# Kernel tuning notes

Hardware: AMD Instinct MI355X
Metric: run time of the kernel (lower is better)

## Reference

```python
import jax, jax.numpy as jnp
import numpy as np

B, S, D, H = 2, 2048, 768, 12
DEPTH = D // H


def setup_inputs() -> dict:
    key = jax.random.key(0)
    ks = jax.random.split(key, 8)
    scale = 1.0 / np.sqrt(D)
    inp = {
        "query": jax.random.normal(ks[0], (B, S, D), jnp.float32),
        "key": jax.random.normal(ks[1], (B, S, D), jnp.float32),
        "value": jax.random.normal(ks[2], (B, S, D), jnp.float32),
        # additive mask convention: 1.0 where attention is disallowed (causal)
        "mask": jnp.triu(jnp.ones((1, 1, S, S), jnp.float32), k=1),
        "Wq": jax.random.normal(ks[3], (D, D), jnp.float32) * scale,
        "bq": jnp.zeros((D,), jnp.float32),
        "Wk": jax.random.normal(ks[4], (D, D), jnp.float32) * scale,
        "bk": jnp.zeros((D,), jnp.float32),
        "Wv": jax.random.normal(ks[5], (D, D), jnp.float32) * scale,
        "bv": jnp.zeros((D,), jnp.float32),
        "Wo": jax.random.normal(ks[6], (D, D), jnp.float32) * scale,
        "bo": jnp.zeros((D,), jnp.float32),
    }
    return inp


def _split_heads(x):
    # [B, S, D] -> [B, H, S, depth]
    b, s, _ = x.shape
    return x.reshape(b, s, H, DEPTH).transpose(0, 2, 1, 3)


def reference(query, key, value, mask, Wq, bq, Wk, bk, Wv, bv, Wo, bo):
    q = _split_heads(query @ Wq + bq)   # [B,H,S,depth]
    k = _split_heads(key @ Wk + bk)
    v = _split_heads(value @ Wv + bv)

    d_k = jnp.asarray(DEPTH, q.dtype)
    logits = jnp.einsum("bhqd,bhkd->bhqk", q, k) / jnp.sqrt(d_k)
    logits = logits + mask * -1e9
    weights = jax.nn.softmax(logits, axis=-1)          # [B,H,S,S] -- O(N^2)
    attn = jnp.einsum("bhqk,bhkd->bhqd", weights, v)    # [B,H,S,depth]

    concat = attn.transpose(0, 2, 1, 3).reshape(query.shape[0], -1, D)
    return concat @ Wo + bo
```

## Files before the change

kernel.cpp:

```cpp
#include <hip/hip_runtime.h>


typedef __bf16 bf16;
typedef __bf16 bf16x8 __attribute__((ext_vector_type(8)));
typedef __bf16 bf16x4 __attribute__((ext_vector_type(4)));
typedef float  f32x4  __attribute__((ext_vector_type(4)));

__device__ __forceinline__ void async_load16(const void* g, void* l) {
  __builtin_amdgcn_global_load_lds(
      (__attribute__((address_space(1))) void*)g,
      (__attribute__((address_space(3))) void*)l, 16, 0, 0);
}

__constant__ unsigned char chunk_tab[40] = {
  3, 4, 5, 6, 7, 8, 9, 10, 11, 12, 13, 14, 15,
  7 | 16, 8 | 16, 9 | 16, 10 | 16, 11 | 16, 12 | 16, 13 | 16, 14 | 16, 15 | 16,
  11 | 32, 12 | 32, 13 | 32, 14 | 32, 15 | 32,
  15 | 48,
  2, 6 | 16, 10 | 32, 14 | 48,
  1, 5 | 16, 9 | 32, 13 | 48,
  0, 4 | 16, 8 | 32, 12 | 48,
};

__global__ __launch_bounds__(256) void convert_kernel(
    const float* __restrict__ q, const float* __restrict__ k,
    const float* __restrict__ v, bf16* __restrict__ qo,
    bf16* __restrict__ ko, bf16* __restrict__ vo) {
  const float* src; bf16* dst;
  if (blockIdx.y == 0)      { src = q; dst = qo; }
  else if (blockIdx.y == 1) { src = k; dst = ko; }
  else                      { src = v; dst = vo; }
  size_t i = ((size_t)blockIdx.x * 256 + threadIdx.x) * 8;
  f32x4 a = *(const f32x4*)(src + i);
  f32x4 b = *(const f32x4*)(src + i + 4);
  bf16x8 o;
  o[0]=(bf16)a[0]; o[1]=(bf16)a[1]; o[2]=(bf16)a[2]; o[3]=(bf16)a[3];
  o[4]=(bf16)b[0]; o[5]=(bf16)b[1]; o[6]=(bf16)b[2]; o[7]=(bf16)b[3];
  *(bf16x8*)(dst + i) = o;
}

__global__ __launch_bounds__(256) void transpose_w_kernel(
    const float* __restrict__ W0, const float* __restrict__ W1,
    const float* __restrict__ W2, const float* __restrict__ W3,
    bf16* __restrict__ T0, bf16* __restrict__ T1,
    bf16* __restrict__ T2, bf16* __restrict__ T3) {
  const float* W; bf16* T;
  switch (blockIdx.z) {
    case 0: W = W0; T = T0; break;
    case 1: W = W1; T = T1; break;
    case 2: W = W2; T = T2; break;
    default: W = W3; T = T3; break;
  }
  __shared__ float tile[32][33];
  const int tx = threadIdx.x, ty = threadIdx.y;
  const int k0 = blockIdx.y * 32, n0 = blockIdx.x * 32;
#pragma unroll
  for (int j = 0; j < 32; j += 8)
    tile[ty + j][tx] = W[(size_t)(k0 + ty + j) * 768 + n0 + tx];
  __syncthreads();
#pragma unroll
  for (int j = 0; j < 32; j += 8) {
    int n = ty + j;
    T[(size_t)(n0 + n) * 768 + k0 + tx] = (bf16)tile[tx][n];
  }
}

__global__ __launch_bounds__(256, 4) void gemm_qkv_kernel(
    const bf16* __restrict__ A0, const bf16* __restrict__ A1, const bf16* __restrict__ A2,
    const bf16* __restrict__ W0, const bf16* __restrict__ W1, const bf16* __restrict__ W2,
    const float* __restrict__ b0, const float* __restrict__ b1, const float* __restrict__ b2,
    bf16* __restrict__ Q, bf16* __restrict__ K, bf16* __restrict__ V) {
  __shared__ __align__(16) char smem[32768];
  const int bidx = blockIdx.x;
  const int xcd = bidx & 7, ii = bidx >> 3;
  const int nt = ii % 6, mzi = ii / 6;
  const int mz = mzi * 8 + xcd;
  const int m = mz & 31, z = mz >> 5;
  const int m0 = m * 128, n0 = nt * 128;

  const bf16* A    = (z == 0) ? A0 : (z == 1) ? A1 : A2;
  const bf16* Wt   = (z == 0) ? W0 : (z == 1) ? W1 : W2;
  const float* bias = (z == 0) ? b0 : (z == 1) ? b1 : b2;
  bf16* outb = (z == 0) ? Q : (z == 1) ? K : V;
  const int mode = (z == 2) ? 1 : 0;

  const int t = threadIdx.x;
  const int w = t >> 6, lane = t & 63;
  const int wm = w >> 1, wn = w & 1;
  const int quad = lane >> 4, l15 = lane & 15;
  const int srow = lane >> 3, k8p = lane & 7;

  size_t offA[4], offB[4];
  int ldsOff[4];
#pragma unroll
  for (int i = 0; i < 4; ++i) {
    const int rl = w * 32 + i * 8 + srow;
    const int kk = k8p ^ (rl & 7);
    offA[i] = (size_t)(m0 + rl) * 768 + kk * 8;
    offB[i] = (size_t)(n0 + rl) * 768 + kk * 8;
    ldsOff[i] = (w * 32 + i * 8) * 128;
  }

  f32x4 acc[4][4] = {};

  for (int kidx = 0; kidx < 12; ++kidx) {
    const int k1 = kidx * 64;
#pragma unroll
    for (int i = 0; i < 4; ++i) {
      async_load16(A  + offA[i] + k1, smem + ldsOff[i]);
      async_load16(Wt + offB[i] + k1, smem + 16384 + ldsOff[i]);
    }
    __syncthreads();
    const bf16* As = (const bf16*)smem;
    const bf16* Bs = (const bf16*)(smem + 16384);
#pragma unroll
    for (int ks = 0; ks < 2; ++ks) {
      bf16x8 af[4], bfv[4];
      const int slot = (((ks * 4 + quad) ^ (lane & 7)) * 8);
#pragma unroll
      for (int mi = 0; mi < 4; ++mi)
        af[mi] = *(const bf16x8*)(As + (wm * 64 + mi * 16 + l15) * 64 + slot);
#pragma unroll
      for (int ni = 0; ni < 4; ++ni)
        bfv[ni] = *(const bf16x8*)(Bs + (wn * 64 + ni * 16 + l15) * 64 + slot);
#pragma unroll
      for (int mi = 0; mi < 4; ++mi)
#pragma unroll
        for (int ni = 0; ni < 4; ++ni)
          acc[mi][ni] = __builtin_amdgcn_mfma_f32_16x16x32_bf16(af[mi], bfv[ni], acc[mi][ni], 0, 0, 0);
    }
    __syncthreads();
  }

#pragma unroll
  for (int ni = 0; ni < 4; ++ni) {
    const float bc = bias[n0 + wn * 64 + ni * 16 + l15];
#pragma unroll
    for (int mi = 0; mi < 4; ++mi)
#pragma unroll
      for (int r = 0; r < 4; ++r) acc[mi][ni][r] += bc;
  }

  if (mode == 0) {
    bf16* Ce = (bf16*)smem;
#pragma unroll
    for (int hh = 0; hh < 2; ++hh) {
      if (wm == hh) {
#pragma unroll
        for (int ni = 0; ni < 4; ++ni) {
          const int col = wn * 64 + ni * 16 + l15;
#pragma unroll
          for (int mi = 0; mi < 4; ++mi) {
            const int row = mi * 16 + quad * 4;
#pragma unroll
            for (int r = 0; r < 4; ++r)
              Ce[(row + r) * 136 + col] = (bf16)acc[mi][ni][r];
          }
        }
      }
      __syncthreads();
#pragma unroll
      for (int j = 0; j < 4; ++j) {
        const int ci = j * 256 + t;
        const int row = ci >> 4, c8 = (ci & 15) * 8;
        bf16x8 vv = *(const bf16x8*)(Ce + row * 136 + c8);
        const int rg = m0 + hh * 64 + row, cg = n0 + c8;
        const int bb = rg >> 11, s = rg & 2047;
        const int h = cg >> 6, d = cg & 63;
        *(bf16x8*)(outb + ((size_t)(bb * 12 + h) * 2048 + s) * 64 + d) = vv;
      }
      __syncthreads();
    }
  } else {
    bf16* Ct = (bf16*)smem;
#pragma unroll
    for (int hh = 0; hh < 2; ++hh) {
      if (wm == hh) {
#pragma unroll
        for (int ni = 0; ni < 4; ++ni) {
          const int col = wn * 64 + ni * 16 + l15;
#pragma unroll
          for (int mi = 0; mi < 4; ++mi) {
            const int row = mi * 16 + quad * 4;
            bf16x4 pv;
            pv[0] = (bf16)acc[mi][ni][0]; pv[1] = (bf16)acc[mi][ni][1];
            pv[2] = (bf16)acc[mi][ni][2]; pv[3] = (bf16)acc[mi][ni][3];
            *(bf16x4*)(Ct + (size_t)col * 72 + row) = pv;
          }
        }
      }
      __syncthreads();
#pragma unroll
      for (int j = 0; j < 4; ++j) {
        const int ci = j * 256 + t;
        const int col = ci >> 3, r8 = (ci & 7) * 8;
        bf16x8 vv = *(const bf16x8*)(Ct + col * 72 + r8);
        const int cg = n0 + col;
        const int h = cg >> 6, d = cg & 63;
        const int rg = m0 + hh * 64 + r8;
        const int bb = rg >> 11, s = rg & 2047;
        *(bf16x8*)(outb + ((size_t)(bb * 12 + h) * 64 + d) * 2048 + s) = vv;
      }
      __syncthreads();
    }
  }
}

__global__ __launch_bounds__(256, 4) void attn_kernel(
    const bf16* __restrict__ Qh, const bf16* __restrict__ Kh,
    const bf16* __restrict__ Vt,
    bf16* __restrict__ O0, bf16* __restrict__ O1,
    bf16* __restrict__ O2, bf16* __restrict__ O3,
    float* __restrict__ L0, float* __restrict__ L1,
    float* __restrict__ L2, float* __restrict__ L3) {
  const int ent = chunk_tab[blockIdx.x / 24];
  const int bh = blockIdx.x % 24;
  const int qt = ent & 15, c = ent >> 4;
  const int q0 = qt * 128;
  const int kt_begin = c * 8;
  const int ntiles = 2 * qt + 2;
  const int kt_end = (kt_begin + 8 < ntiles) ? kt_begin + 8 : ntiles;

  __shared__ __align__(16) char smem[32768];
  bf16* Ps = (bf16*)(smem + 16384);

  const int t = threadIdx.x;
  const int w = t >> 6, lane = t & 63, quad = lane >> 4, l15 = lane & 15;
  const int srow = lane >> 3, k8p = lane & 7;
  const bf16* Qp = Qh + (size_t)bh * (2048 * 64);
  const bf16* Kp = Kh + (size_t)bh * (2048 * 64);
  const bf16* Vp = Vt + (size_t)bh * (64 * 2048);

  size_t offK[2], offV[2];
  int ldsOff[2];
#pragma unroll
  for (int i = 0; i < 2; ++i) {
    const int rl = w * 16 + i * 8 + srow;
    const int kk = k8p ^ (rl & 7);
    offK[i] = (size_t)rl * 64 + kk * 8;
    offV[i] = (size_t)rl * 2048 + kk * 8;
    ldsOff[i] = (w * 16 + i * 8) * 128;
  }

  bf16x8 qf[2][2];
#pragma unroll
  for (int mi = 0; mi < 2; ++mi)
#pragma unroll
    for (int ks = 0; ks < 2; ++ks) {
      const int qrow = q0 + w * 32 + mi * 16 + l15;
      qf[mi][ks] = *(const bf16x8*)(Qp + (size_t)qrow * 64 + ks * 32 + quad * 8);
    }

  f32x4 o[2][4] = {};
  float lp[2] = {0.f, 0.f};
  const float sc = 0.125f * 1.44269504f;

  for (int kt = kt_begin; kt < kt_end; ++kt) {
    const int k0 = kt * 64;
#pragma unroll
    for (int i = 0; i < 2; ++i) {
      async_load16(Kp + offK[i] + (size_t)k0 * 64, smem + ldsOff[i]);
      async_load16(Vp + offV[i] + k0,              smem + 8192 + ldsOff[i]);
    }
    __syncthreads();
    const bf16* Ks = (const bf16*)smem;
    const bf16* Vs = (const bf16*)(smem + 8192);

    f32x4 st[4][2] = {};
#pragma unroll
    for (int ks = 0; ks < 2; ++ks) {
      const int slot = (((ks * 4 + quad) ^ (lane & 7)) * 8);
      bf16x8 kf[4];
#pragma unroll
      for (int ni = 0; ni < 4; ++ni)
        kf[ni] = *(const bf16x8*)(Ks + (ni * 16 + l15) * 64 + slot);
#pragma unroll
      for (int ni = 0; ni < 4; ++ni)
#pragma unroll
        for (int mi = 0; mi < 2; ++mi)
          st[ni][mi] = __builtin_amdgcn_mfma_f32_16x16x32_bf16(kf[ni], qf[mi][ks], st[ni][mi], 0, 0, 0);
    }

    const bool diag = (k0 + 63 > q0);
#pragma unroll
    for (int mi = 0; mi < 2; ++mi) {
      const int q_local = w * 32 + mi * 16 + l15;
      const int qg = q0 + q_local;
#pragma unroll
      for (int ni = 0; ni < 4; ++ni) {
        bf16x4 pv;
#pragma unroll
        for (int r = 0; r < 4; ++r) {
          float p = __builtin_amdgcn_exp2f(st[ni][mi][r] * sc);
          if (diag && (k0 + ni * 16 + quad * 4 + r > qg)) p = 0.0f;
          lp[mi] += p;
          pv[r] = (bf16)p;
        }
        const int cc = ni * 2 + (quad >> 1);
        *(bf16x4*)(Ps + q_local * 64 + ((cc ^ (q_local & 7)) << 3) + ((quad & 1) << 2)) = pv;
      }
    }

#pragma unroll
    for (int ks = 0; ks < 2; ++ks) {
      const int slot = (((ks * 4 + quad) ^ (lane & 7)) * 8);
      bf16x8 pf[2], vfr[4];
#pragma unroll
      for (int mi = 0; mi < 2; ++mi)
        pf[mi] = *(const bf16x8*)(Ps + (w * 32 + mi * 16 + l15) * 64 + slot);
#pragma unroll
      for (int di = 0; di < 4; ++di)
        vfr[di] = *(const bf16x8*)(Vs + (di * 16 + l15) * 64 + slot);
#pragma unroll
      for (int mi = 0; mi < 2; ++mi)
#pragma unroll
        for (int di = 0; di < 4; ++di)
          o[mi][di] = __builtin_amdgcn_mfma_f32_16x16x32_bf16(pf[mi], vfr[di], o[mi][di], 0, 0, 0);
    }
    __syncthreads();
  }

  bf16* Op; float* Lp_;
  switch (c) {
    case 0: Op = O0; Lp_ = L0; break;
    case 1: Op = O1; Lp_ = L1; break;
    case 2: Op = O2; Lp_ = L2; break;
    default: Op = O3; Lp_ = L3; break;
  }
  const int rows_c = 2048 - 512 * c;
  const size_t rbase = (size_t)bh * rows_c + (q0 - 512 * c);

#pragma unroll
  for (int mi = 0; mi < 2; ++mi) {
    float l = lp[mi];
    l += __shfl_xor(l, 16);
    l += __shfl_xor(l, 32);
    if (quad == 0) Lp_[rbase + w * 32 + mi * 16 + l15] = l;
#pragma unroll
    for (int di = 0; di < 4; ++di) {
      const int d = di * 16 + l15;
#pragma unroll
      for (int r = 0; r < 4; ++r) {
        const size_t row = rbase + w * 32 + mi * 16 + quad * 4 + r;
        Op[row * 64 + d] = (bf16)o[mi][di][r];
      }
    }
  }
}

__global__ __launch_bounds__(256) void lsum_kernel(
    const float* __restrict__ L0, const float* __restrict__ L1,
    const float* __restrict__ L2, const float* __restrict__ L3,
    float* __restrict__ Linv) {
  const int row = blockIdx.x * 256 + threadIdx.x;
  const int bh = row >> 11, s = row & 2047;
  float l = L0[row];
  if (s >= 512)  l += L1[(size_t)bh * 1536 + (s - 512)];
  if (s >= 1024) l += L2[(size_t)bh * 1024 + (s - 1024)];
  if (s >= 1536) l += L3[(size_t)bh * 512  + (s - 1536)];
  Linv[row] = 1.0f / l;
}

__global__ __launch_bounds__(256, 4) void gemm_out_kernel(
    const bf16* __restrict__ O0, const bf16* __restrict__ O1,
    const bf16* __restrict__ O2, const bf16* __restrict__ O3,
    const float* __restrict__ Linv, const bf16* __restrict__ Wt,
    const float* __restrict__ bias, float* __restrict__ out) {
  __shared__ __align__(16) char smem[24576];
  const int bidx = blockIdx.x;
  const int xcd = bidx & 7, ii = bidx >> 3;
  const int nt = ii % 6, mg = ii / 6;
  const int mt = mg * 8 + xcd;
  const int m0 = mt * 64, n0 = nt * 128;
  const int bb = mt >> 5;
  const int s0 = (mt & 31) * 64;
  const int nch = 1 + (s0 >= 512) + (s0 >= 1024) + (s0 >= 1536);

  const int t = threadIdx.x;
  const int w = t >> 6, lane = t & 63;
  const int wm = w >> 1, wn = w & 1;
  const int quad = lane >> 4, l15 = lane & 15;
  const int srow = lane >> 3, k8p = lane & 7;

  size_t offB[4]; int ldsOffB[4];
#pragma unroll
  for (int i = 0; i < 4; ++i) {
    const int rl = w * 32 + i * 8 + srow;
    const int kk = k8p ^ (rl & 7);
    offB[i] = (size_t)(n0 + rl) * 768 + kk * 8;
    ldsOffB[i] = (w * 32 + i * 8) * 128;
  }
  const int arow = t >> 2;
  const int ac2 = (t & 3) * 2;
  const int sA = s0 + arow;
  size_t ro0[2], ro1[2], ro2[2], ro3[2];
  int apos[2];
#pragma unroll
  for (int j = 0; j < 2; ++j) {
    const int cch = ac2 + j;
    ro0[j] = (size_t)sA * 64 + cch * 8;
    ro1[j] = (size_t)(sA - 512) * 64 + cch * 8;
    ro2[j] = (size_t)(sA - 1024) * 64 + cch * 8;
    ro3[j] = (size_t)(sA - 1536) * 64 + cch * 8;
    apos[j] = arow * 64 + ((cch ^ (arow & 7)) << 3);
  }

  f32x4 acc[2][4] = {};
  bf16x8 pa0[2], pa1[2], pa2[2], pa3[2];
  float lv;

  auto loadA = [&](int kk) {
    const size_t bh = (size_t)(bb * 12 + kk);
    lv = Linv[bh * 2048 + sA];
#pragma unroll
    for (int j = 0; j < 2; ++j) pa0[j] = *(const bf16x8*)(O0 + bh * 131072 + ro0[j]);
    if (nch >= 2)
#pragma unroll
      for (int j = 0; j < 2; ++j) pa1[j] = *(const bf16x8*)(O1 + bh * 98304 + ro1[j]);
    if (nch >= 3)
#pragma unroll
      for (int j = 0; j < 2; ++j) pa2[j] = *(const bf16x8*)(O2 + bh * 65536 + ro2[j]);
    if (nch >= 4)
#pragma unroll
      for (int j = 0; j < 2; ++j) pa3[j] = *(const bf16x8*)(O3 + bh * 32768 + ro3[j]);
  };
  auto writeA = [&]() {
    bf16* As = (bf16*)smem;
#pragma unroll
    for (int j = 0; j < 2; ++j) {
      float f[8];
#pragma unroll
      for (int k = 0; k < 8; ++k) f[k] = (float)pa0[j][k];
      if (nch >= 2)
#pragma unroll
        for (int k = 0; k < 8; ++k) f[k] += (float)pa1[j][k];
      if (nch >= 3)
#pragma unroll
        for (int k = 0; k < 8; ++k) f[k] += (float)pa2[j][k];
      if (nch >= 4)
#pragma unroll
        for (int k = 0; k < 8; ++k) f[k] += (float)pa3[j][k];
      bf16x8 o;
#pragma unroll
      for (int k = 0; k < 8; ++k) o[k] = (bf16)(f[k] * lv);
      *(bf16x8*)(As + apos[j]) = o;
    }
  };

  loadA(0);
  for (int kidx = 0; kidx < 12; ++kidx) {
    writeA();
    const int k1 = kidx * 64;
#pragma unroll
    for (int i = 0; i < 4; ++i)
      async_load16(Wt + offB[i] + k1, smem + 8192 + ldsOffB[i]);
    __syncthreads();
    if (kidx < 11) loadA(kidx + 1);
    const bf16* As = (const bf16*)smem;
    const bf16* Bs = (const bf16*)(smem + 8192);
#pragma unroll
    for (int ks = 0; ks < 2; ++ks) {
      bf16x8 af[2], bfv[4];
      const int slot = (((ks * 4 + quad) ^ (lane & 7)) * 8);
#pragma unroll
      for (int mi = 0; mi < 2; ++mi)
        af[mi] = *(const bf16x8*)(As + (wm * 32 + mi * 16 + l15) * 64 + slot);
#pragma unroll
      for (int ni = 0; ni < 4; ++ni)
        bfv[ni] = *(const bf16x8*)(Bs + (wn * 64 + ni * 16 + l15) * 64 + slot);
#pragma unroll
      for (int mi = 0; mi < 2; ++mi)
#pragma unroll
        for (int ni = 0; ni < 4; ++ni)
          acc[mi][ni] = __builtin_amdgcn_mfma_f32_16x16x32_bf16(af[mi], bfv[ni], acc[mi][ni], 0, 0, 0);
    }
    __syncthreads();
  }

#pragma unroll
  for (int ni = 0; ni < 4; ++ni) {
    const float bc = bias[n0 + wn * 64 + ni * 16 + l15];
#pragma unroll
    for (int mi = 0; mi < 2; ++mi)
#pragma unroll
      for (int r = 0; r < 4; ++r) acc[mi][ni][r] += bc;
  }

#pragma unroll
  for (int ni = 0; ni < 4; ++ni) {
    const int col = n0 + wn * 64 + ni * 16 + l15;
#pragma unroll
    for (int mi = 0; mi < 2; ++mi) {
      const int row = m0 + wm * 32 + mi * 16 + quad * 4;
#pragma unroll
      for (int r = 0; r < 4; ++r)
        out[(size_t)(row + r) * 768 + col] = acc[mi][ni][r];
    }
  }
}

extern "C" void kernel_launch(void* const* d_in, const int* in_sizes, int n_in,
                              void* d_out, int out_size, void* d_ws, size_t ws_size,
                              hipStream_t stream) {
  const float* query = (const float*)d_in[0];
  const float* key   = (const float*)d_in[1];
  const float* value = (const float*)d_in[2];
  const float* Wq = (const float*)d_in[4];
  const float* bq = (const float*)d_in[5];
  const float* Wk = (const float*)d_in[6];
  const float* bk = (const float*)d_in[7];
  const float* Wv = (const float*)d_in[8];
  const float* bv = (const float*)d_in[9];
  const float* Wo = (const float*)d_in[10];
  const float* bo = (const float*)d_in[11];
  float* out = (float*)d_out;

  char* ws = (char*)d_ws;
  bf16* qb   = (bf16*)(ws);
  bf16* kb   = (bf16*)(ws + 6291456);
  bf16* vb   = (bf16*)(ws + 12582912);
  bf16* O0   = (bf16*)(ws);
  bf16* O1   = (bf16*)(ws + 6291456);
  bf16* O2   = (bf16*)(ws + 11010048);
  bf16* O3   = (bf16*)(ws + 14155776);
  float* L0  = (float*)(ws + 15728640);
  float* L1  = (float*)(ws + 15925248);
  float* L2  = (float*)(ws + 16072704);
  float* L3  = (float*)(ws + 16171008);
  float* Liv = (float*)(ws + 16220160);
  bf16* wtq  = (bf16*)(ws + 18874368);
  bf16* wtk  = (bf16*)(ws + 20054016);
  bf16* wtv  = (bf16*)(ws + 21233664);
  bf16* wto  = (bf16*)(ws + 22413312);
  bf16* Qh   = (bf16*)(ws + 23592960);
  bf16* Kh   = (bf16*)(ws + 29884416);
  bf16* Vtb  = (bf16*)(ws + 36175872);

  convert_kernel<<<dim3(1536, 3), 256, 0, stream>>>(query, key, value, qb, kb, vb);
  transpose_w_kernel<<<dim3(24, 24, 4), dim3(32, 8), 0, stream>>>(Wq, Wk, Wv, Wo, wtq, wtk, wtv, wto);
  gemm_qkv_kernel<<<dim3(576), 256, 0, stream>>>(qb, kb, vb, wtq, wtk, wtv, bq, bk, bv, Qh, Kh, Vtb);
  attn_kernel<<<dim3(960), 256, 0, stream>>>(Qh, Kh, Vtb, O0, O1, O2, O3, L0, L1, L2, L3);
  lsum_kernel<<<dim3(192), 256, 0, stream>>>(L0, L1, L2, L3, Liv);
  gemm_out_kernel<<<dim3(384), 256, 0, stream>>>(O0, O1, O2, O3, Liv, wto, bo, out);
}
```

Baseline: 189.2 us.

## Fuse input conversion into QKV GEMM and row-sum into output GEMM

Removes the separate fp32→bf16 convert kernel by having the QKV GEMM load fp32 activations into registers and convert them while writing to LDS, with register prefetch of the next K tile. Likewise removes the lsum kernel by computing inverse row sums into shared memory at the start of the output GEMM. Replaces the async global-to-LDS loads with register-staged loads plus software prefetch in the GEMMs and the attention kernel. This cuts two launches and an intermediate round trip through memory, at the cost of more registers (occupancy hint lowered to 3) and more VALU conversion work inside the GEMM.

```diff
diff --git a/kernel.cpp b/kernel.cpp
--- a/kernel.cpp
+++ b/kernel.cpp
@@ -5,12 +5,6 @@
 typedef __bf16 bf16x8 __attribute__((ext_vector_type(8)));
 typedef __bf16 bf16x4 __attribute__((ext_vector_type(4)));
 typedef float  f32x4  __attribute__((ext_vector_type(4)));
-
-__device__ __forceinline__ void async_load16(const void* g, void* l) {
-  __builtin_amdgcn_global_load_lds(
-      (__attribute__((address_space(1))) void*)g,
-      (__attribute__((address_space(3))) void*)l, 16, 0, 0);
-}
 
 __constant__ unsigned char chunk_tab[40] = {
   3, 4, 5, 6, 7, 8, 9, 10, 11, 12, 13, 14, 15,
@@ -21,23 +15,6 @@
   1, 5 | 16, 9 | 32, 13 | 48,
   0, 4 | 16, 8 | 32, 12 | 48,
 };
-
-__global__ __launch_bounds__(256) void convert_kernel(
-    const float* __restrict__ q, const float* __restrict__ k,
-    const float* __restrict__ v, bf16* __restrict__ qo,
-    bf16* __restrict__ ko, bf16* __restrict__ vo) {
-  const float* src; bf16* dst;
-  if (blockIdx.y == 0)      { src = q; dst = qo; }
-  else if (blockIdx.y == 1) { src = k; dst = ko; }
-  else                      { src = v; dst = vo; }
-  size_t i = ((size_t)blockIdx.x * 256 + threadIdx.x) * 8;
-  f32x4 a = *(const f32x4*)(src + i);
-  f32x4 b = *(const f32x4*)(src + i + 4);
-  bf16x8 o;
-  o[0]=(bf16)a[0]; o[1]=(bf16)a[1]; o[2]=(bf16)a[2]; o[3]=(bf16)a[3];
-  o[4]=(bf16)b[0]; o[5]=(bf16)b[1]; o[6]=(bf16)b[2]; o[7]=(bf16)b[3];
-  *(bf16x8*)(dst + i) = o;
-}
 
 __global__ __launch_bounds__(256) void transpose_w_kernel(
     const float* __restrict__ W0, const float* __restrict__ W1,
@@ -65,8 +42,8 @@
   }
 }
 
-__global__ __launch_bounds__(256, 4) void gemm_qkv_kernel(
-    const bf16* __restrict__ A0, const bf16* __restrict__ A1, const bf16* __restrict__ A2,
+__global__ __launch_bounds__(256, 3) void gemm_qkv_kernel(
+    const float* __restrict__ X0, const float* __restrict__ X1, const float* __restrict__ X2,
     const bf16* __restrict__ W0, const bf16* __restrict__ W1, const bf16* __restrict__ W2,
     const float* __restrict__ b0, const float* __restrict__ b1, const float* __restrict__ b2,
     bf16* __restrict__ Q, bf16* __restrict__ K, bf16* __restrict__ V) {
@@ -78,8 +55,8 @@
   const int m = mz & 31, z = mz >> 5;
   const int m0 = m * 128, n0 = nt * 128;
 
-  const bf16* A    = (z == 0) ? A0 : (z == 1) ? A1 : A2;
-  const bf16* Wt   = (z == 0) ? W0 : (z == 1) ? W1 : W2;
+  const float* A    = (z == 0) ? X0 : (z == 1) ? X1 : X2;
+  const bf16* Wt    = (z == 0) ? W0 : (z == 1) ? W1 : W2;
   const float* bias = (z == 0) ? b0 : (z == 1) ? b1 : b2;
   bf16* outb = (z == 0) ? Q : (z == 1) ? K : V;
   const int mode = (z == 2) ? 1 : 0;
@@ -90,29 +67,57 @@
   const int quad = lane >> 4, l15 = lane & 15;
   const int srow = lane >> 3, k8p = lane & 7;
 
-  size_t offA[4], offB[4];
-  int ldsOff[4];
+  size_t offB[4]; int ldsB[4];
 #pragma unroll
   for (int i = 0; i < 4; ++i) {
     const int rl = w * 32 + i * 8 + srow;
     const int kk = k8p ^ (rl & 7);
-    offA[i] = (size_t)(m0 + rl) * 768 + kk * 8;
     offB[i] = (size_t)(n0 + rl) * 768 + kk * 8;
-    ldsOff[i] = (w * 32 + i * 8) * 128;
+    ldsB[i] = 8192 + (w * 32 + i * 8) * 64 + lane * 8;
+  }
+  const int arow0 = t >> 3;
+  const int ac = t & 7;
+  size_t offA[4]; int aposA[4];
+#pragma unroll
+  for (int i = 0; i < 4; ++i) {
+    const int row = arow0 + i * 32;
+    offA[i] = (size_t)(m0 + row) * 768 + ac * 8;
+    aposA[i] = row * 64 + ((ac ^ (row & 7)) << 3);
   }
 
   f32x4 acc[4][4] = {};
-
+  f32x4 pa[4], pb[4];
+  bf16x8 pw[4];
+
+  auto loadAB = [&](int k1) {
+#pragma unroll
+    for (int i = 0; i < 4; ++i) {
+      pa[i] = *(const f32x4*)(A + offA[i] + k1);
+      pb[i] = *(const f32x4*)(A + offA[i] + k1 + 4);
+    }
+#pragma unroll
+    for (int i = 0; i < 4; ++i)
+      pw[i] = *(const bf16x8*)(Wt + offB[i] + k1);
+  };
+  auto writeAB = [&]() {
+    bf16* As = (bf16*)smem;
+#pragma unroll
+    for (int i = 0; i < 4; ++i) {
+      bf16x8 o;
+      o[0]=(bf16)pa[i][0]; o[1]=(bf16)pa[i][1]; o[2]=(bf16)pa[i][2]; o[3]=(bf16)pa[i][3];
+      o[4]=(bf16)pb[i][0]; o[5]=(bf16)pb[i][1]; o[6]=(bf16)pb[i][2]; o[7]=(bf16)pb[i][3];
+      *(bf16x8*)(As + aposA[i]) = o;
+      *(bf16x8*)(As + ldsB[i]) = pw[i];
+    }
+  };
+
+  loadAB(0);
   for (int kidx = 0; kidx < 12; ++kidx) {
-    const int k1 = kidx * 64;
-#pragma unroll
-    for (int i = 0; i < 4; ++i) {
-      async_load16(A  + offA[i] + k1, smem + ldsOff[i]);
-      async_load16(Wt + offB[i] + k1, smem + 16384 + ldsOff[i]);
-    }
+    writeAB();
     __syncthreads();
+    if (kidx < 11) loadAB((kidx + 1) * 64);
     const bf16* As = (const bf16*)smem;
-    const bf16* Bs = (const bf16*)(smem + 16384);
+    const bf16* Bs = (const bf16*)smem + 8192;
 #pragma unroll
     for (int ks = 0; ks < 2; ++ks) {
       bf16x8 af[4], bfv[4];
@@ -232,14 +237,15 @@
   const bf16* Vp = Vt + (size_t)bh * (64 * 2048);
 
   size_t offK[2], offV[2];
-  int ldsOff[2];
+  int ldsK[2], ldsV[2];
 #pragma unroll
   for (int i = 0; i < 2; ++i) {
     const int rl = w * 16 + i * 8 + srow;
     const int kk = k8p ^ (rl & 7);
     offK[i] = (size_t)rl * 64 + kk * 8;
     offV[i] = (size_t)rl * 2048 + kk * 8;
-    ldsOff[i] = (w * 16 + i * 8) * 128;
+    ldsK[i] = (w * 16 + i * 8) * 64 + lane * 8;
+    ldsV[i] = 4096 + (w * 16 + i * 8) * 64 + lane * 8;
   }
 
   bf16x8 qf[2][2];
@@ -255,16 +261,28 @@
   float lp[2] = {0.f, 0.f};
   const float sc = 0.125f * 1.44269504f;
 
+  bf16x8 kreg[2], vreg[2];
+  auto loadKV = [&](int kb) {
+#pragma unroll
+    for (int i = 0; i < 2; ++i) {
+      kreg[i] = *(const bf16x8*)(Kp + offK[i] + (size_t)kb * 64);
+      vreg[i] = *(const bf16x8*)(Vp + offV[i] + kb);
+    }
+  };
+
+  loadKV(kt_begin * 64);
   for (int kt = kt_begin; kt < kt_end; ++kt) {
     const int k0 = kt * 64;
+    bf16* sw = (bf16*)smem;
 #pragma unroll
     for (int i = 0; i < 2; ++i) {
-      async_load16(Kp + offK[i] + (size_t)k0 * 64, smem + ldsOff[i]);
-      async_load16(Vp + offV[i] + k0,              smem + 8192 + ldsOff[i]);
+      *(bf16x8*)(sw + ldsK[i]) = kreg[i];
+      *(bf16x8*)(sw + ldsV[i]) = vreg[i];
     }
     __syncthreads();
+    if (kt + 1 < kt_end) loadKV((kt + 1) * 64);
     const bf16* Ks = (const bf16*)smem;
-    const bf16* Vs = (const bf16*)(smem + 8192);
+    const bf16* Vs = (const bf16*)smem + 4096;
 
     f32x4 st[4][2] = {};
 #pragma unroll
@@ -348,25 +366,15 @@
   }
 }
 
-__global__ __launch_bounds__(256) void lsum_kernel(
-    const float* __restrict__ L0, const float* __restrict__ L1,
-    const float* __restrict__ L2, const float* __restrict__ L3,
-    float* __restrict__ Linv) {
-  const int row = blockIdx.x * 256 + threadIdx.x;
-  const int bh = row >> 11, s = row & 2047;
-  float l = L0[row];
-  if (s >= 512)  l += L1[(size_t)bh * 1536 + (s - 512)];
-  if (s >= 1024) l += L2[(size_t)bh * 1024 + (s - 1024)];
-  if (s >= 1536) l += L3[(size_t)bh * 512  + (s - 1536)];
-  Linv[row] = 1.0f / l;
-}
-
 __global__ __launch_bounds__(256, 4) void gemm_out_kernel(
     const bf16* __restrict__ O0, const bf16* __restrict__ O1,
     const bf16* __restrict__ O2, const bf16* __restrict__ O3,
-    const float* __restrict__ Linv, const bf16* __restrict__ Wt,
-    const float* __restrict__ bias, float* __restrict__ out) {
-  __shared__ __align__(16) char smem[24576];
+    const float* __restrict__ L0, const float* __restrict__ L1,
+    const float* __restrict__ L2, const float* __restrict__ L3,
+    const bf16* __restrict__ Wt, const float* __restrict__ bias,
+    float* __restrict__ out) {
+  __shared__ __align__(16) char smem[27648];
+  float* LivS = (float*)(smem + 24576);
   const int bidx = blockIdx.x;
   const int xcd = bidx & 7, ii = bidx >> 3;
   const int nt = ii % 6, mg = ii / 6;
@@ -382,19 +390,30 @@
   const int quad = lane >> 4, l15 = lane & 15;
   const int srow = lane >> 3, k8p = lane & 7;
 
-  size_t offB[4]; int ldsOffB[4];
+  for (int idx = t; idx < 768; idx += 256) {
+    const int kk = idx >> 6, r = idx & 63;
+    const int s = s0 + r;
+    const size_t bh = (size_t)(bb * 12 + kk);
+    float l = L0[bh * 2048 + s];
+    if (s >= 512)  l += L1[bh * 1536 + (s - 512)];
+    if (s >= 1024) l += L2[bh * 1024 + (s - 1024)];
+    if (s >= 1536) l += L3[bh * 512  + (s - 1536)];
+    LivS[idx] = 1.0f / l;
+  }
+
+  size_t offB[4]; int ldsB[4];
 #pragma unroll
   for (int i = 0; i < 4; ++i) {
     const int rl = w * 32 + i * 8 + srow;
     const int kk = k8p ^ (rl & 7);
     offB[i] = (size_t)(n0 + rl) * 768 + kk * 8;
-    ldsOffB[i] = (w * 32 + i * 8) * 128;
+    ldsB[i] = 4096 + (w * 32 + i * 8) * 64 + lane * 8;
   }
   const int arow = t >> 2;
   const int ac2 = (t & 3) * 2;
   const int sA = s0 + arow;
   size_t ro0[2], ro1[2], ro2[2], ro3[2];
-  int apos[2];
+  int aposA[2];
 #pragma unroll
   for (int j = 0; j < 2; ++j) {
     const int cch = ac2 + j;
@@ -402,16 +421,16 @@
     ro1[j] = (size_t)(sA - 512) * 64 + cch * 8;
     ro2[j] = (size_t)(sA - 1024) * 64 + cch * 8;
     ro3[j] = (size_t)(sA - 1536) * 64 + cch * 8;
-    apos[j] = arow * 64 + ((cch ^ (arow & 7)) << 3);
+    aposA[j] = arow * 64 + ((cch ^ (arow & 7)) << 3);
   }
 
   f32x4 acc[2][4] = {};
-  bf16x8 pa0[2], pa1[2], pa2[2], pa3[2];
-  float lv;
-
-  auto loadA = [&](int kk) {
+  bf16x8 pa0[2], pa1[2], pa2[2], pa3[2], pw[4];
+  int kkcur = 0;
+
+  auto loadAB = [&](int kk) {
+    kkcur = kk;
     const size_t bh = (size_t)(bb * 12 + kk);
-    lv = Linv[bh * 2048 + sA];
 #pragma unroll
     for (int j = 0; j < 2; ++j) pa0[j] = *(const bf16x8*)(O0 + bh * 131072 + ro0[j]);
     if (nch >= 2)
@@ -423,9 +442,13 @@
     if (nch >= 4)
 #pragma unroll
       for (int j = 0; j < 2; ++j) pa3[j] = *(const bf16x8*)(O3 + bh * 32768 + ro3[j]);
+#pragma unroll
+    for (int i = 0; i < 4; ++i)
+      pw[i] = *(const bf16x8*)(Wt + offB[i] + kk * 64);
   };
-  auto writeA = [&]() {
+  auto writeAB = [&]() {
     bf16* As = (bf16*)smem;
+    const float lv = LivS[kkcur * 64 + arow];
 #pragma unroll
     for (int j = 0; j < 2; ++j) {
       float f[8];
@@ -443,21 +466,21 @@
       bf16x8 o;
 #pragma unroll
       for (int k = 0; k < 8; ++k) o[k] = (bf16)(f[k] * lv);
-      *(bf16x8*)(As + apos[j]) = o;
-    }
+      *(bf16x8*)(As + aposA[j]) = o;
+    }
+#pragma unroll
+    for (int i = 0; i < 4; ++i)
+      *(bf16x8*)(As + ldsB[i]) = pw[i];
   };
 
-  loadA(0);
+  loadAB(0);
+  __syncthreads();
   for (int kidx = 0; kidx < 12; ++kidx) {
-    writeA();
-    const int k1 = kidx * 64;
-#pragma unroll
-    for (int i = 0; i < 4; ++i)
-      async_load16(Wt + offB[i] + k1, smem + 8192 + ldsOffB[i]);
+    writeAB();
     __syncthreads();
-    if (kidx < 11) loadA(kidx + 1);
+    if (kidx < 11) loadAB(kidx + 1);
     const bf16* As = (const bf16*)smem;
-    const bf16* Bs = (const bf16*)(smem + 8192);
+    const bf16* Bs = (const bf16*)smem + 4096;
 #pragma unroll
     for (int ks = 0; ks < 2; ++ks) {
       bf16x8 af[2], bfv[4];
@@ -516,9 +539,6 @@
   float* out = (float*)d_out;
 
   char* ws = (char*)d_ws;
-  bf16* qb   = (bf16*)(ws);
-  bf16* kb   = (bf16*)(ws + 6291456);
-  bf16* vb   = (bf16*)(ws + 12582912);
   bf16* O0   = (bf16*)(ws);
   bf16* O1   = (bf16*)(ws + 6291456);
   bf16* O2   = (bf16*)(ws + 11010048);
@@ -527,19 +547,16 @@
   float* L1  = (float*)(ws + 15925248);
   float* L2  = (float*)(ws + 16072704);
   float* L3  = (float*)(ws + 16171008);
-  float* Liv = (float*)(ws + 16220160);
-  bf16* wtq  = (bf16*)(ws + 18874368);
-  bf16* wtk  = (bf16*)(ws + 20054016);
-  bf16* wtv  = (bf16*)(ws + 21233664);
-  bf16* wto  = (bf16*)(ws + 22413312);
-  bf16* Qh   = (bf16*)(ws + 23592960);
-  bf16* Kh   = (bf16*)(ws + 29884416);
-  bf16* Vtb  = (bf16*)(ws + 36175872);
-
-  convert_kernel<<<dim3(1536, 3), 256, 0, stream>>>(query, key, value, qb, kb, vb);
+  bf16* wtq  = (bf16*)(ws + 16220160);
+  bf16* wtk  = (bf16*)(ws + 17399808);
+  bf16* wtv  = (bf16*)(ws + 18579456);
+  bf16* wto  = (bf16*)(ws + 19759104);
+  bf16* Qh   = (bf16*)(ws + 20938752);
+  bf16* Kh   = (bf16*)(ws + 27230208);
+  bf16* Vtb  = (bf16*)(ws + 33521664);
+
   transpose_w_kernel<<<dim3(24, 24, 4), dim3(32, 8), 0, stream>>>(Wq, Wk, Wv, Wo, wtq, wtk, wtv, wto);
-  gemm_qkv_kernel<<<dim3(576), 256, 0, stream>>>(qb, kb, vb, wtq, wtk, wtv, bq, bk, bv, Qh, Kh, Vtb);
+  gemm_qkv_kernel<<<dim3(576), 256, 0, stream>>>(query, key, value, wtq, wtk, wtv, bq, bk, bv, Qh, Kh, Vtb);
   attn_kernel<<<dim3(960), 256, 0, stream>>>(Qh, Kh, Vtb, O0, O1, O2, O3, L0, L1, L2, L3);
-  lsum_kernel<<<dim3(192), 256, 0, stream>>>(L0, L1, L2, L3, Liv);
-  gemm_out_kernel<<<dim3(384), 256, 0, stream>>>(O0, O1, O2, O3, Liv, wto, bo, out);
+  gemm_out_kernel<<<dim3(384), 256, 0, stream>>>(O0, O1, O2, O3, L0, L1, L2, L3, wto, bo, out);
 }
```

Measured after the change: 225.4 us. +19.1%, slower.
